# Optimization experiments

Measured on AMD Instinct MI355X. Metric: run time of the kernel, lower is better.

Reference implementation:

```python
import jax, jax.numpy as jnp
import numpy as np

# --- model hyperparameters (match init_kwargs / TrajectoryDecoder defaults) ---
R, T, KREG = 3, 16, 8          # num_radii, num_theta, reg_dim
RADIUS = 40.0                  # radius_scale
VEHICLE_HIDDEN = 16
MAP_HIDDEN = 8
IN_CH = VEHICLE_HIDDEN + MAP_HIDDEN  # 24
PREDICT_WINDOW = 30
TWO_PI = 2.0 * np.pi


def _reg_roll(f):
    # f: [..., C, k] -> [..., C, k(l), k(m)] with entry f[..., c, (m-l)%k]
    m = jnp.arange(KREG)[None, :]
    l = jnp.arange(KREG)[:, None]
    return f[..., (m - l) % KREG]


def _equilinear(W, f):
    # equivariant linear map between regular reps = circular (group) conv over reg dim
    # W: [out, in, k], f: [..., in, k] -> [..., out, k]
    return jnp.einsum('oil,...ilm->...om', W, _reg_roll(f))


def _reg2rho1(f, w):
    # frequency-1 Fourier projection of the regular rep -> rho1 (2-vector); 2 free params
    ang = TWO_PI * jnp.arange(KREG) / KREG
    c, s = jnp.cos(ang), jnp.sin(ang)
    W2 = jnp.stack([w[0] * c - w[1] * s, w[0] * s + w[1] * c], axis=-1)  # [k, 2]
    return jnp.einsum('...cm,md->...cd', f, W2)


def _cts_aggregate(dst_p, src_p, H, src_mask):
    # Continuous conv aggregation: bilinear interpolation of a polar-binned kernel
    # already contracted with source features.
    # H: [B, S, R, T, O, k] per-source, per-(radius,theta)-bin transformed features
    B, S, O = src_p.shape[0], src_p.shape[1], H.shape[-2]
    rel = src_p[:, None, :, :] - dst_p[:, :, None, :]      # [B, Nd, S, 2]
    d = jnp.sqrt(jnp.sum(rel * rel, axis=-1) + 1e-12)      # [B, Nd, S]
    valid = (d < RADIUS).astype(dst_p.dtype) * src_mask[:, None, :]
    win = jnp.maximum(1.0 - (d / RADIUS) ** 2, 0.0) ** 3   # CConv window
    cnt = jnp.maximum(jnp.sum(valid, axis=-1, keepdims=True), 1.0)
    base_w = valid * win / cnt
    # radial interpolation (clamped linear)
    u = jnp.clip(d / RADIUS, 0.0, 1.0) * (R - 1)
    r0f = jnp.floor(u); wr = u - r0f
    r0 = r0f.astype(jnp.int32); r1 = jnp.minimum(r0 + 1, R - 1)
    # angular interpolation (circular linear)
    t = ((jnp.arctan2(rel[..., 1], rel[..., 0]) / TWO_PI) % 1.0) * T
    t0f = jnp.floor(t); wt = t - t0f
    t0 = t0f.astype(jnp.int32) % T; t1 = (t0 + 1) % T
    Hf = H.reshape(B, S, R * T, O, KREG)
    bidx = jnp.arange(B)[:, None, None]
    sidx = jnp.arange(S)[None, None, :]
    out = jnp.zeros((B, dst_p.shape[1], O, KREG), dtype=dst_p.dtype)
    for ri, ti, cw in ((r0, t0, (1 - wr) * (1 - wt)),
                       (r0, t1, (1 - wr) * wt),
                       (r1, t0, wr * (1 - wt)),
                       (r1, t1, wr * wt)):
        g = Hf[bidx, sidx, ri * T + ti]                    # [B, Nd, S, O, k] irregular gather
        out = out + jnp.einsum('bns,bnsok->bnok', base_w * cw, g)
    return out


def _conv_reg(K, src_p, dst_p, f, src_mask):
    # EquiCtsConv2dRegToReg: per-bin group conv over reg dim, then continuous-conv gather
    H = jnp.einsum('rtoil,bsilm->bsrtom', K, _reg_roll(f))
    return _cts_aggregate(dst_p, src_p, H, src_mask)


def _conv_rho1(K, src_p, dst_p, v, src_mask):
    # EquiCtsConv2dRho1ToReg (in_channels=1): contract 2-vector input per bin
    H = jnp.einsum('rtomd,bsd->bsrtom', K, v)
    return _cts_aggregate(dst_p, src_p, H, src_mask)


def _decode(p, feat, car_mask, K_vehicle, Wd_vehicle, K_conv1, Wd1, K_conv2, Wd2):
    out = _conv_reg(K_vehicle, p, p, feat, car_mask) + _equilinear(Wd_vehicle, feat)
    for K, Wd in ((K_conv1, Wd1), (K_conv2, Wd2)):
        inf = jax.nn.relu(out)
        oc = _conv_reg(K, p, p, inf, car_mask)
        od = _equilinear(Wd, inf)
        out = oc + od + out if od.shape[-2] == out.shape[-2] else oc + od
    return jax.nn.relu(out)


def _forward(p, feat, map_p, map_feat, car_mask, map_mask,
             K_vehicle, Wd_vehicle, K_conv1, Wd1, K_conv2, Wd2,
             Wd_back, w_rho1, K_map):
    outputs = []
    output = _decode(p, feat, car_mask, K_vehicle, Wd_vehicle, K_conv1, Wd1, K_conv2, Wd2)
    delta = _reg2rho1(output, w_rho1)                      # [B, N, 3, 2]
    outputs.append(delta.at[..., 0, :].add(p))
    for _ in range(1, PREDICT_WINDOW):
        p = p + delta[..., 0, :]
        back = jnp.tanh(_equilinear(Wd_back, output))      # [B, N, 16, k]
        feat_v = feat[..., :VEHICLE_HIDDEN, :] * back
        enc = jax.nn.relu(_conv_rho1(K_map, map_p, p, map_feat, map_mask))  # MapEncoder
        feat = jnp.concatenate([feat_v, enc], axis=-2)     # [B, N, 24, k]
        output = _decode(p, feat, car_mask, K_vehicle, Wd_vehicle, K_conv1, Wd1, K_conv2, Wd2)
        delta = _reg2rho1(output, w_rho1)
        outputs.append(delta.at[..., 0, :].add(p))
    return jnp.stack(outputs, axis=0)                      # [30, B, N, 3, 2]


def setup_inputs() -> dict:
    key = jax.random.key(0)
    ks = jax.random.split(key, 13)
    B, N, M = 8, 64, 1024
    sc = 0.1
    return {
        'p': jax.random.normal(ks[0], (B, N, 2)) * 20.0,
        'feat': jax.random.normal(ks[1], (B, N, IN_CH, KREG)),
        'map_p': jax.random.normal(ks[2], (B, M, 2)) * 20.0,
        'map_feat': jax.random.normal(ks[3], (B, M, 2)),
        'car_mask': jnp.ones((B, N), dtype=jnp.float32),
        'map_mask': jnp.ones((B, M), dtype=jnp.float32),
        'K_vehicle': jax.random.normal(ks[4], (R, T, 8, IN_CH, KREG)) * sc,
        'Wd_vehicle': jax.random.normal(ks[5], (8, IN_CH, KREG)) * sc,
        'K_conv1': jax.random.normal(ks[6], (R, T, 8, 8, KREG)) * sc,
        'Wd1': jax.random.normal(ks[7], (8, 8, KREG)) * sc,
        'K_conv2': jax.random.normal(ks[8], (R, T, 3, 8, KREG)) * sc,
        'Wd2': jax.random.normal(ks[9], (3, 8, KREG)) * sc,
        'Wd_back': jax.random.normal(ks[10], (VEHICLE_HIDDEN, 3, KREG)) * sc,
        'w_rho1': jax.random.normal(ks[11], (2,)) * sc,
        'K_map': jax.random.normal(ks[12], (R, T, MAP_HIDDEN, KREG, 2)) * sc,
    }


def reference(p, feat, map_p, map_feat, car_mask, map_mask,
              K_vehicle, Wd_vehicle, K_conv1, Wd1, K_conv2, Wd2,
              Wd_back, w_rho1, K_map):
    return _forward(p, feat, map_p, map_feat, car_mask, map_mask,
                    K_vehicle, Wd_vehicle, K_conv1, Wd1, K_conv2, Wd2,
                    Wd_back, w_rho1, K_map)
```

## Files before the change

### kernel.cpp

```cpp
#include <hip/hip_runtime.h>
#include <math.h>

#define NB 8
#define NV 64
#define NM 1024
#define NR 3
#define NT 16
#define KR 8
#define RTOT 48
#define RADIUSF 40.0f
#define TWO_PIF 6.283185307179586f

__device__ __forceinline__ void pair_geom(float relx, float rely, float mask,
                                          float& valid, float& win,
                                          int bin[4], float cw[4]) {
    float d = sqrtf(relx * relx + rely * rely + 1e-12f);
    valid = (d < RADIUSF) ? mask : 0.0f;
    float q = d * (1.0f / RADIUSF);
    float w1 = fmaxf(1.0f - q * q, 0.0f);
    win = w1 * w1 * w1;
    float u = fminf(fmaxf(q, 0.0f), 1.0f) * (float)(NR - 1);
    float r0f = floorf(u);
    float wr = u - r0f;
    int r0 = (int)r0f;
    int r1 = min(r0 + 1, NR - 1);
    float a = atan2f(rely, relx) * (1.0f / TWO_PIF);
    a = a - floorf(a);
    float t = a * (float)NT;
    float t0f = floorf(t);
    float wt = t - t0f;
    int t0 = ((int)t0f) & (NT - 1);
    int t1 = (t0 + 1) & (NT - 1);
    bin[0] = r0 * NT + t0; cw[0] = (1.0f - wr) * (1.0f - wt);
    bin[1] = r0 * NT + t1; cw[1] = (1.0f - wr) * wt;
    bin[2] = r1 * NT + t0; cw[2] = wr * (1.0f - wt);
    bin[3] = r1 * NT + t1; cw[3] = wr * wt;
}

__global__ __launch_bounds__(64) void k_pairs0(const float* __restrict__ p,
                                               const float* __restrict__ car_mask,
                                               float* __restrict__ w4,
                                               int* __restrict__ bin4) {
    int b = blockIdx.x >> 6, n = blockIdx.x & 63;
    int s = threadIdx.x;
    float dx = p[(b * NV + n) * 2 + 0], dy = p[(b * NV + n) * 2 + 1];
    float relx = p[(b * NV + s) * 2 + 0] - dx;
    float rely = p[(b * NV + s) * 2 + 1] - dy;
    float valid, win; int bin[4]; float cw[4];
    pair_geom(relx, rely, car_mask[b * NV + s], valid, win, bin, cw);
    float c = valid;
#pragma unroll
    for (int off = 32; off > 0; off >>= 1) c += __shfl_xor(c, off);
    float bw = valid * win / fmaxf(c, 1.0f);
    int base = (blockIdx.x * NV + s) * 4;
#pragma unroll
    for (int q = 0; q < 4; ++q) { w4[base + q] = bw * cw[q]; bin4[base + q] = bin[q]; }
}

__global__ __launch_bounds__(256) void k_trans(
        const float* __restrict__ Kv, const float* __restrict__ K1g,
        const float* __restrict__ K2g, float4* __restrict__ KTv,
        float4* __restrict__ KT1, float4* __restrict__ KT2) {
    int idx = blockIdx.x * 256 + threadIdx.x;
    if (idx < 48 * 384) {
        int j = idx / 384, p = idx % 384;
        KTv[idx] = *(const float4*)(Kv + p * 192 + j * 4);
    } else if (idx < 48 * 384 + 16 * 384) {
        int r = idx - 48 * 384;
        int j = r / 384, p = r % 384;
        KT1[r] = *(const float4*)(K1g + p * 64 + j * 4);
    } else if (idx < 48 * 384 + 16 * 384 + 16 * 144) {
        int r = idx - (48 * 384 + 16 * 384);
        int j = r / 144, p = r % 144;
        KT2[r] = *(const float4*)(K2g + p * 64 + j * 4);
    }
}

__global__ __launch_bounds__(256) void k_H0(const float* __restrict__ inb,
        const float4* __restrict__ KT, float* __restrict__ H) {
    __shared__ __align__(16) float s_f[192];
    int bs = blockIdx.x, tid = threadIdx.x;
    if (tid < 192) s_f[tid] = inb[bs * 192 + tid];
    __syncthreads();
    for (int p = tid; p < 384; p += 256) {
        float acc[KR];
#pragma unroll
        for (int m = 0; m < KR; ++m) acc[m] = 0.f;
#pragma unroll 8
        for (int i = 0; i < 24; ++i) {
            float4 k0 = KT[(2 * i) * 384 + p];
            float4 k1 = KT[(2 * i + 1) * 384 + p];
            float kk[8] = {k0.x, k0.y, k0.z, k0.w, k1.x, k1.y, k1.z, k1.w};
            float ff[8];
            *(float4*)&ff[0] = *(const float4*)&s_f[i * 8];
            *(float4*)&ff[4] = *(const float4*)&s_f[i * 8 + 4];
#pragma unroll
            for (int l = 0; l < KR; ++l) {
                float kl = kk[l];
#pragma unroll
                for (int m = 0; m < KR; ++m)
                    acc[m] = fmaf(kl, ff[(m - l) & 7], acc[m]);
            }
        }
        int rt = p >> 3, o = p & 7;
        float* hr = H + (size_t)(bs * RTOT + rt) * 64 + o * KR;
#pragma unroll
        for (int m = 0; m < KR; ++m) hr[m] = acc[m];
    }
}

__global__ __launch_bounds__(256) void k_advHv(int t,
        const float* __restrict__ pprev, float* __restrict__ pcur,
        const float* __restrict__ outD, float* __restrict__ feat,
        const float* __restrict__ w_rho1, const float* __restrict__ WdBack,
        const float* __restrict__ Kmap, const float* __restrict__ map_p,
        const float* __restrict__ map_feat, const float* __restrict__ map_mask,
        const float* __restrict__ car_mask,
        float* __restrict__ w4, int* __restrict__ bin4,
        float* __restrict__ out,
        const float4* __restrict__ KTv, float* __restrict__ Hv) {
    __shared__ float s_out0[NV * KR];
    __shared__ float s_own[3 * KR];
    __shared__ float s_psrc[NV * 2];
    __shared__ float s_G4[4 * 96];
    __shared__ float s_G[96];
    __shared__ float s_wred[4];
    __shared__ float s_w2[KR * 2];
    __shared__ __align__(16) float s_f2[192];

    int tid = threadIdx.x;
    int bn = blockIdx.x, b = bn >> 6, n = bn & 63;

    for (int i = tid; i < NV * KR; i += 256)
        s_out0[i] = outD[(b * NV + (i >> 3)) * 24 + (i & 7)];
    if (tid < 24) s_own[tid] = outD[(b * NV + n) * 24 + tid];
    if (tid >= 32 && tid < 48) {
        int r = tid - 32, m = r >> 1, dd = r & 1;
        float ang = TWO_PIF * (float)m / (float)KR;
        float sn, cs; sincosf(ang, &sn, &cs);
        float w0 = w_rho1[0], wq = w_rho1[1];
        s_w2[r] = (dd == 0) ? (w0 * cs - wq * sn) : (w0 * sn + wq * cs);
    }
    if (tid < 96) { s_G4[tid] = 0.f; s_G4[96 + tid] = 0.f; s_G4[192 + tid] = 0.f; s_G4[288 + tid] = 0.f; }
    __syncthreads();

    if (tid < NV) {
        int s = tid;
        float dx0 = 0.0f, dy0 = 0.0f;
#pragma unroll
        for (int m = 0; m < KR; ++m) {
            float v = s_out0[s * KR + m];
            dx0 = fmaf(v, s_w2[m * 2 + 0], dx0);
            dy0 = fmaf(v, s_w2[m * 2 + 1], dy0);
        }
        s_psrc[s * 2 + 0] = pprev[(b * NV + s) * 2 + 0] + dx0;
        s_psrc[s * 2 + 1] = pprev[(b * NV + s) * 2 + 1] + dy0;
    }
    if (tid >= 64 && tid < 70) {
        int r = tid - 64, c = r >> 1, dd = r & 1;
        float acc = 0.0f;
#pragma unroll
        for (int m = 0; m < KR; ++m)
            acc = fmaf(s_own[c * KR + m], s_w2[m * 2 + dd], acc);
        if (c == 0) acc += pprev[(b * NV + n) * 2 + dd];
        out[(((t - 1) * NB + b) * NV + n) * 6 + c * 2 + dd] = acc;
    }
    __syncthreads();
    if (tid < 2) pcur[(b * NV + n) * 2 + tid] = s_psrc[n * 2 + tid];

    float pdx = s_psrc[n * 2 + 0], pdy = s_psrc[n * 2 + 1];

    if (tid < NV) {
        int s = tid;
        float valid, win; int bin[4]; float cw[4];
        pair_geom(s_psrc[s * 2 + 0] - pdx, s_psrc[s * 2 + 1] - pdy,
                  car_mask[b * NV + s], valid, win, bin, cw);
        float c = valid;
#pragma unroll
        for (int off = 32; off > 0; off >>= 1) c += __shfl_xor(c, off);
        float bw = valid * win / fmaxf(c, 1.0f);
        int base = (bn * NV + s) * 4;
#pragma unroll
        for (int q = 0; q < 4; ++q) { w4[base + q] = bw * cw[q]; bin4[base + q] = bin[q]; }
    }

    float lc = 0.0f;
    float* myG = &s_G4[(tid >> 6) * 96];
#pragma unroll
    for (int j = 0; j < NM / 256; ++j) {
        int s = tid + j * 256;
        float2 mp = *(const float2*)&map_p[(b * NM + s) * 2];
        float valid, win; int bin[4]; float cw[4];
        pair_geom(mp.x - pdx, mp.y - pdy, map_mask[b * NM + s], valid, win, bin, cw);
        lc += valid;
        float ww = valid * win;
        if (ww > 0.0f) {
            float2 f2 = *(const float2*)&map_feat[(b * NM + s) * 2];
#pragma unroll
            for (int q = 0; q < 4; ++q) {
                float w = ww * cw[q];
                atomicAdd(&myG[bin[q] * 2 + 0], w * f2.x);
                atomicAdd(&myG[bin[q] * 2 + 1], w * f2.y);
            }
        }
    }
#pragma unroll
    for (int off = 32; off > 0; off >>= 1) lc += __shfl_xor(lc, off);
    if ((tid & 63) == 0) s_wred[tid >> 6] = lc;
    __syncthreads();
    if (tid < 96) s_G[tid] = s_G4[tid] + s_G4[96 + tid] + s_G4[192 + tid] + s_G4[288 + tid];
    __syncthreads();
    float invc = 1.0f / fmaxf(s_wred[0] + s_wred[1] + s_wred[2] + s_wred[3], 1.0f);

    if (tid < 64) {
        float acc = 0.0f;
#pragma unroll 8
        for (int rt = 0; rt < RTOT; ++rt) {
            float2 k2 = *(const float2*)&Kmap[(rt * 64 + tid) * 2];
            acc = fmaf(k2.x, s_G[rt * 2 + 0], acc);
            acc = fmaf(k2.y, s_G[rt * 2 + 1], acc);
        }
        s_f2[128 + tid] = fmaxf(acc * invc, 0.0f);
    }
    if (tid >= 128) {
        int r = tid - 128, i = r >> 3, m = r & 7;
        float acc = 0.0f;
#pragma unroll
        for (int c = 0; c < 3; ++c)
#pragma unroll
            for (int l = 0; l < KR; ++l)
                acc = fmaf(WdBack[(i * 3 + c) * 8 + l], s_own[c * 8 + ((m - l) & 7)], acc);
        s_f2[r] = feat[(b * NV + n) * 192 + r] * tanhf(acc);
    }
    __syncthreads();
    if (tid < 192) feat[bn * 192 + tid] = s_f2[tid];

    for (int p = tid; p < 384; p += 256) {
        float acc[KR];
#pragma unroll
        for (int m = 0; m < KR; ++m) acc[m] = 0.f;
#pragma unroll 8
        for (int i = 0; i < 24; ++i) {
            float4 k0 = KTv[(2 * i) * 384 + p];
            float4 k1 = KTv[(2 * i + 1) * 384 + p];
            float kk[8] = {k0.x, k0.y, k0.z, k0.w, k1.x, k1.y, k1.z, k1.w};
            float ff[8];
            *(float4*)&ff[0] = *(const float4*)&s_f2[i * 8];
            *(float4*)&ff[4] = *(const float4*)&s_f2[i * 8 + 4];
#pragma unroll
            for (int l = 0; l < KR; ++l) {
                float kl = kk[l];
#pragma unroll
                for (int m = 0; m < KR; ++m)
                    acc[m] = fmaf(kl, ff[(m - l) & 7], acc[m]);
            }
        }
        int rt = p >> 3, o = p & 7;
        float* hr = Hv + (size_t)(bn * RTOT + rt) * 64 + o * KR;
#pragma unroll
        for (int m = 0; m < KR; ++m) hr[m] = acc[m];
    }
}

template<int ICH, bool RELU_IN, bool RESID, int OCH2>
__global__ __launch_bounds__(256) void k_aggH(const float* __restrict__ inb,
        const float* __restrict__ H, const float* __restrict__ Wd,
        const float* __restrict__ w4, const int* __restrict__ bin4,
        const float4* __restrict__ KT2, float* __restrict__ outb,
        float* __restrict__ Hout) {
    constexpr int NC = ICH * KR;
    constexpr int HS = 64;
    constexpr int NPAIR2 = RTOT * OCH2;
    constexpr int HS2 = OCH2 * KR;
    __shared__ float s_w[256];
    __shared__ int   s_row[256];
    __shared__ float s_in[NC];
    __shared__ __align__(16) float s_part[16 * HS];
    __shared__ __align__(16) float s_f2[HS];
    int tid = threadIdx.x, bn = blockIdx.x, b = bn >> 6;
    s_w[tid] = w4[bn * 256 + tid];
    s_row[tid] = (b * NV + (tid >> 2)) * RTOT + bin4[bn * 256 + tid];
    if (tid < NC) s_in[tid] = inb[bn * NC + tid];
    __syncthreads();
    {
        int w = tid >> 6, lane = tid & 63;
        int g = lane >> 4, c4 = lane & 15;
        float4 acc = make_float4(0.f, 0.f, 0.f, 0.f);
#pragma unroll
        for (int j = 0; j < 16; ++j) {
            int idx = w * 64 + j * 4 + g;
            float we = s_w[idx];
            float4 v = *(const float4*)&H[(size_t)s_row[idx] * HS + c4 * 4];
            acc.x = fmaf(we, v.x, acc.x);
            acc.y = fmaf(we, v.y, acc.y);
            acc.z = fmaf(we, v.z, acc.z);
            acc.w = fmaf(we, v.w, acc.w);
        }
        *(float4*)&s_part[(w * 4 + g) * HS + c4 * 4] = acc;
    }
    __syncthreads();
    if (tid < HS) {
        float tot = 0.f;
#pragma unroll
        for (int k = 0; k < 16; ++k) tot += s_part[k * HS + tid];
        int o = tid / KR, m = tid & 7;
#pragma unroll
        for (int i = 0; i < ICH; ++i) {
            const float* Wr = Wd + (o * ICH + i) * KR;
#pragma unroll
            for (int l = 0; l < KR; ++l) {
                float v = s_in[i * KR + ((m - l) & 7)];
                if (RELU_IN) v = fmaxf(v, 0.f);
                tot = fmaf(Wr[l], v, tot);
            }
        }
        if (RESID) tot += s_in[tid];
        outb[bn * HS + tid] = tot;
        s_f2[tid] = fmaxf(tot, 0.f);
    }
    __syncthreads();
    for (int p = tid; p < NPAIR2; p += 256) {
        float acc2[KR];
#pragma unroll
        for (int m = 0; m < KR; ++m) acc2[m] = 0.f;
#pragma unroll 4
        for (int i = 0; i < 8; ++i) {
            float4 k0 = KT2[(2 * i) * NPAIR2 + p];
            float4 k1 = KT2[(2 * i + 1) * NPAIR2 + p];
            float kk[8] = {k0.x, k0.y, k0.z, k0.w, k1.x, k1.y, k1.z, k1.w};
            float ff[8];
            *(float4*)&ff[0] = *(const float4*)&s_f2[i * 8];
            *(float4*)&ff[4] = *(const float4*)&s_f2[i * 8 + 4];
#pragma unroll
            for (int l = 0; l < KR; ++l) {
                float kl = kk[l];
#pragma unroll
                for (int m = 0; m < KR; ++m)
                    acc2[m] = fmaf(kl, ff[(m - l) & 7], acc2[m]);
            }
        }
        int rt = p / OCH2, o = p - rt * OCH2;
        float* hr = Hout + (size_t)(bn * RTOT + rt) * HS2 + o * KR;
#pragma unroll
        for (int m = 0; m < KR; ++m) hr[m] = acc2[m];
    }
}

__global__ __launch_bounds__(256) void k_agg3(const float* __restrict__ inb,
        const float* __restrict__ H, const float* __restrict__ Wd,
        const float* __restrict__ w4, const int* __restrict__ bin4,
        float* __restrict__ outb) {
    constexpr int NC = 64;
    constexpr int HS = 24;
    __shared__ float s_w[256];
    __shared__ int   s_row[256];
    __shared__ float s_in[NC];
    __shared__ __align__(16) float s_part[32 * HS];
    int tid = threadIdx.x, bn = blockIdx.x, b = bn >> 6;
    s_w[tid] = w4[bn * 256 + tid];
    s_row[tid] = (b * NV + (tid >> 2)) * RTOT + bin4[bn * 256 + tid];
    if (tid < NC) s_in[tid] = inb[bn * NC + tid];
    __syncthreads();
    {
        int w = tid >> 6, lane = tid & 63;
        int g = lane >> 3, c4 = lane & 7;
        float4 acc = make_float4(0.f, 0.f, 0.f, 0.f);
#pragma unroll
        for (int j = 0; j < 8; ++j) {
            int idx = w * 64 + j * 8 + g;
            float we = s_w[idx];
            if (c4 < 6) {
                float4 v = *(const float4*)&H[(size_t)s_row[idx] * HS + c4 * 4];
                acc.x = fmaf(we, v.x, acc.x);
                acc.y = fmaf(we, v.y, acc.y);
                acc.z = fmaf(we, v.z, acc.z);
                acc.w = fmaf(we, v.w, acc.w);
            }
        }
        if (c4 < 6) *(float4*)&s_part[(w * 8 + g) * HS + c4 * 4] = acc;
    }
    __syncthreads();
    if (tid < HS) {
        float tot = 0.f;
#pragma unroll
        for (int k = 0; k < 32; ++k) tot += s_part[k * HS + tid];
        int o = tid / KR, m = tid & 7;
#pragma unroll
        for (int i = 0; i < 8; ++i) {
            const float* Wr = Wd + (o * 8 + i) * KR;
#pragma unroll
            for (int l = 0; l < KR; ++l)
                tot = fmaf(Wr[l], fmaxf(s_in[i * KR + ((m - l) & 7)], 0.f), tot);
        }
        outb[bn * HS + tid] = fmaxf(tot, 0.f);
    }
}

__global__ void k_final(const float* __restrict__ outD, const float* __restrict__ pcur,
                        const float* __restrict__ w_rho1, float* __restrict__ out) {
    int idx = blockIdx.x * blockDim.x + threadIdx.x;
    if (idx >= NB * NV * 6) return;
    int bn = idx / 6, r = idx % 6, c = r >> 1, dd = r & 1;
    float w0 = w_rho1[0], wq = w_rho1[1];
    float acc = 0.0f;
#pragma unroll
    for (int m = 0; m < KR; ++m) {
        float ang = TWO_PIF * (float)m / (float)KR;
        float sn, cs; sincosf(ang, &sn, &cs);
        float w2 = (dd == 0) ? (w0 * cs - wq * sn) : (w0 * sn + wq * cs);
        acc = fmaf(outD[bn * 24 + c * 8 + m], w2, acc);
    }
    if (c == 0) acc += pcur[bn * 2 + dd];
    out[(29 * NB * NV + bn) * 6 + r] = acc;
}

extern "C" void kernel_launch(void* const* d_in, const int* in_sizes, int n_in,
                              void* d_out, int out_size, void* d_ws, size_t ws_size,
                              hipStream_t stream) {
    const float* in_p     = (const float*)d_in[0];
    const float* in_feat  = (const float*)d_in[1];
    const float* map_p    = (const float*)d_in[2];
    const float* map_feat = (const float*)d_in[3];
    const float* car_mask = (const float*)d_in[4];
    const float* map_mask = (const float*)d_in[5];
    const float* Kv       = (const float*)d_in[6];
    const float* WdV      = (const float*)d_in[7];
    const float* K1       = (const float*)d_in[8];
    const float* Wd1      = (const float*)d_in[9];
    const float* K2       = (const float*)d_in[10];
    const float* Wd2      = (const float*)d_in[11];
    const float* WdBack   = (const float*)d_in[12];
    const float* w_rho1   = (const float*)d_in[13];
    const float* Kmap     = (const float*)d_in[14];

    float* ws   = (float*)d_ws;
    float* pbuf0 = ws;
    float* pbuf1 = ws + 1024;
    float* feat  = ws + 2048;
    float* out1  = ws + 100352;
    float* out2  = ws + 133120;
    float* outD  = ws + 165888;
    float* w4    = ws + 178176;
    int*   bin4  = (int*)(ws + 309248);
    float4* KTv  = (float4*)(ws + 440320);
    float4* KT1  = (float4*)(ws + 514048);
    float4* KT2  = (float4*)(ws + 538624);
    float* Hv    = ws + 547840;
    float* H1    = ws + 2120704;
    float* H2    = ws + 3693568;
    float* out   = (float*)d_out;

    hipMemcpyAsync(pbuf0, in_p, NB * NV * 2 * sizeof(float),
                   hipMemcpyDeviceToDevice, stream);
    hipMemcpyAsync(feat, in_feat, NB * NV * 24 * KR * sizeof(float),
                   hipMemcpyDeviceToDevice, stream);

    k_trans<<<105, 256, 0, stream>>>(Kv, K1, K2, KTv, KT1, KT2);
    k_pairs0<<<NB * NV, 64, 0, stream>>>(pbuf0, car_mask, w4, bin4);

    auto decode = [&]() {
        k_aggH<24, false, false, 8><<<NB * NV, 256, 0, stream>>>(feat, Hv, WdV, w4, bin4, KT1, out1, H1);
        k_aggH<8, true, true, 3><<<NB * NV, 256, 0, stream>>>(out1, H1, Wd1, w4, bin4, KT2, out2, H2);
        k_agg3<<<NB * NV, 256, 0, stream>>>(out2, H2, Wd2, w4, bin4, outD);
    };

    k_H0<<<NB * NV, 256, 0, stream>>>(feat, KTv, Hv);
    decode();
    for (int t = 1; t < 30; ++t) {
        float* pprev = (t & 1) ? pbuf0 : pbuf1;
        float* pcur  = (t & 1) ? pbuf1 : pbuf0;
        k_advHv<<<NB * NV, 256, 0, stream>>>(t, pprev, pcur, outD, feat,
                                             w_rho1, WdBack, Kmap, map_p, map_feat,
                                             map_mask, car_mask, w4, bin4, out,
                                             KTv, Hv);
        decode();
    }
    k_final<<<12, 256, 0, stream>>>(outD, pbuf1, w_rho1, out);
}
```

Measured before the change: 1.765 ms.

## Fuse stage-3 aggregation into advance kernel and pair geometry into first decode stage

After: 1.744 ms. Within noise of the previous version (-1.2%).

```diff
diff --git a/kernel.cpp b/kernel.cpp
--- a/kernel.cpp
+++ b/kernel.cpp
@@ -37,26 +37,6 @@
     bin[3] = r1 * NT + t1; cw[3] = wr * wt;
 }
 
-__global__ __launch_bounds__(64) void k_pairs0(const float* __restrict__ p,
-                                               const float* __restrict__ car_mask,
-                                               float* __restrict__ w4,
-                                               int* __restrict__ bin4) {
-    int b = blockIdx.x >> 6, n = blockIdx.x & 63;
-    int s = threadIdx.x;
-    float dx = p[(b * NV + n) * 2 + 0], dy = p[(b * NV + n) * 2 + 1];
-    float relx = p[(b * NV + s) * 2 + 0] - dx;
-    float rely = p[(b * NV + s) * 2 + 1] - dy;
-    float valid, win; int bin[4]; float cw[4];
-    pair_geom(relx, rely, car_mask[b * NV + s], valid, win, bin, cw);
-    float c = valid;
-#pragma unroll
-    for (int off = 32; off > 0; off >>= 1) c += __shfl_xor(c, off);
-    float bw = valid * win / fmaxf(c, 1.0f);
-    int base = (blockIdx.x * NV + s) * 4;
-#pragma unroll
-    for (int q = 0; q < 4; ++q) { w4[base + q] = bw * cw[q]; bin4[base + q] = bin[q]; }
-}
-
 __global__ __launch_bounds__(256) void k_trans(
         const float* __restrict__ Kv, const float* __restrict__ K1g,
         const float* __restrict__ K2g, float4* __restrict__ KTv,
@@ -109,33 +89,35 @@
     }
 }
 
-__global__ __launch_bounds__(256) void k_advHv(int t,
-        const float* __restrict__ pprev, float* __restrict__ pcur,
-        const float* __restrict__ outD, float* __restrict__ feat,
+__global__ __launch_bounds__(256) void k_A(int t,
+        float* __restrict__ p, const float* __restrict__ out2buf,
+        const float* __restrict__ H2, const float* __restrict__ Wd2,
+        const float* __restrict__ w4, const int* __restrict__ bin4,
+        float* __restrict__ feat,
         const float* __restrict__ w_rho1, const float* __restrict__ WdBack,
         const float* __restrict__ Kmap, const float* __restrict__ map_p,
         const float* __restrict__ map_feat, const float* __restrict__ map_mask,
-        const float* __restrict__ car_mask,
-        float* __restrict__ w4, int* __restrict__ bin4,
-        float* __restrict__ out,
-        const float4* __restrict__ KTv, float* __restrict__ Hv) {
-    __shared__ float s_out0[NV * KR];
-    __shared__ float s_own[3 * KR];
-    __shared__ float s_psrc[NV * 2];
+        const float4* __restrict__ KTv, float* __restrict__ Hv,
+        float* __restrict__ out) {
+    __shared__ float s_w[256];
+    __shared__ int   s_row[256];
+    __shared__ float s_in[64];
+    __shared__ __align__(16) float s_part[32 * 24];
+    __shared__ float s_oD[24];
+    __shared__ float s_w2[16];
     __shared__ float s_G4[4 * 96];
     __shared__ float s_G[96];
     __shared__ float s_wred[4];
-    __shared__ float s_w2[KR * 2];
     __shared__ __align__(16) float s_f2[192];
 
-    int tid = threadIdx.x;
-    int bn = blockIdx.x, b = bn >> 6, n = bn & 63;
-
-    for (int i = tid; i < NV * KR; i += 256)
-        s_out0[i] = outD[(b * NV + (i >> 3)) * 24 + (i & 7)];
-    if (tid < 24) s_own[tid] = outD[(b * NV + n) * 24 + tid];
-    if (tid >= 32 && tid < 48) {
-        int r = tid - 32, m = r >> 1, dd = r & 1;
+    int tid = threadIdx.x, bn = blockIdx.x, b = bn >> 6, n = bn & 63;
+    float2 pold = *(const float2*)&p[bn * 2];
+
+    s_w[tid] = w4[bn * 256 + tid];
+    s_row[tid] = (b * NV + (tid >> 2)) * RTOT + bin4[bn * 256 + tid];
+    if (tid < 64) s_in[tid] = out2buf[bn * 64 + tid];
+    if (tid >= 224 && tid < 240) {
+        int r = tid - 224, m = r >> 1, dd = r & 1;
         float ang = TWO_PIF * (float)m / (float)KR;
         float sn, cs; sincosf(ang, &sn, &cs);
         float w0 = w_rho1[0], wq = w_rho1[1];
@@ -144,47 +126,61 @@
     if (tid < 96) { s_G4[tid] = 0.f; s_G4[96 + tid] = 0.f; s_G4[192 + tid] = 0.f; s_G4[288 + tid] = 0.f; }
     __syncthreads();
 
-    if (tid < NV) {
-        int s = tid;
-        float dx0 = 0.0f, dy0 = 0.0f;
-#pragma unroll
-        for (int m = 0; m < KR; ++m) {
-            float v = s_out0[s * KR + m];
-            dx0 = fmaf(v, s_w2[m * 2 + 0], dx0);
-            dy0 = fmaf(v, s_w2[m * 2 + 1], dy0);
-        }
-        s_psrc[s * 2 + 0] = pprev[(b * NV + s) * 2 + 0] + dx0;
-        s_psrc[s * 2 + 1] = pprev[(b * NV + s) * 2 + 1] + dy0;
-    }
-    if (tid >= 64 && tid < 70) {
-        int r = tid - 64, c = r >> 1, dd = r & 1;
-        float acc = 0.0f;
+    {
+        int w = tid >> 6, lane = tid & 63;
+        int g = lane >> 3, c4 = lane & 7;
+        float4 acc = make_float4(0.f, 0.f, 0.f, 0.f);
+#pragma unroll
+        for (int j = 0; j < 8; ++j) {
+            int idx = w * 64 + j * 8 + g;
+            float we = s_w[idx];
+            if (c4 < 6) {
+                float4 v = *(const float4*)&H2[(size_t)s_row[idx] * 24 + c4 * 4];
+                acc.x = fmaf(we, v.x, acc.x);
+                acc.y = fmaf(we, v.y, acc.y);
+                acc.z = fmaf(we, v.z, acc.z);
+                acc.w = fmaf(we, v.w, acc.w);
+            }
+        }
+        if (c4 < 6) *(float4*)&s_part[(w * 8 + g) * 24 + c4 * 4] = acc;
+    }
+    __syncthreads();
+    if (tid < 24) {
+        float tot = 0.f;
+#pragma unroll
+        for (int k = 0; k < 32; ++k) tot += s_part[k * 24 + tid];
+        int o = tid / KR, m = tid & 7;
+#pragma unroll
+        for (int i = 0; i < 8; ++i) {
+            const float* Wr = Wd2 + (o * 8 + i) * KR;
+#pragma unroll
+            for (int l = 0; l < KR; ++l)
+                tot = fmaf(Wr[l], fmaxf(s_in[i * KR + ((m - l) & 7)], 0.f), tot);
+        }
+        s_oD[tid] = fmaxf(tot, 0.f);
+    }
+    __syncthreads();
+
+    float dx0 = 0.f, dy0 = 0.f;
+#pragma unroll
+    for (int m = 0; m < KR; ++m) {
+        float v = s_oD[m];
+        dx0 = fmaf(v, s_w2[m * 2 + 0], dx0);
+        dy0 = fmaf(v, s_w2[m * 2 + 1], dy0);
+    }
+    if (tid < 6) {
+        int c = tid >> 1, dd = tid & 1;
+        float acc = 0.f;
 #pragma unroll
         for (int m = 0; m < KR; ++m)
-            acc = fmaf(s_own[c * KR + m], s_w2[m * 2 + dd], acc);
-        if (c == 0) acc += pprev[(b * NV + n) * 2 + dd];
-        out[(((t - 1) * NB + b) * NV + n) * 6 + c * 2 + dd] = acc;
-    }
-    __syncthreads();
-    if (tid < 2) pcur[(b * NV + n) * 2 + tid] = s_psrc[n * 2 + tid];
-
-    float pdx = s_psrc[n * 2 + 0], pdy = s_psrc[n * 2 + 1];
-
-    if (tid < NV) {
-        int s = tid;
-        float valid, win; int bin[4]; float cw[4];
-        pair_geom(s_psrc[s * 2 + 0] - pdx, s_psrc[s * 2 + 1] - pdy,
-                  car_mask[b * NV + s], valid, win, bin, cw);
-        float c = valid;
-#pragma unroll
-        for (int off = 32; off > 0; off >>= 1) c += __shfl_xor(c, off);
-        float bw = valid * win / fmaxf(c, 1.0f);
-        int base = (bn * NV + s) * 4;
-#pragma unroll
-        for (int q = 0; q < 4; ++q) { w4[base + q] = bw * cw[q]; bin4[base + q] = bin[q]; }
-    }
-
-    float lc = 0.0f;
+            acc = fmaf(s_oD[c * KR + m], s_w2[m * 2 + dd], acc);
+        if (c == 0) acc += (dd ? pold.y : pold.x);
+        out[(((t - 1) * NB + b) * NV + n) * 6 + tid] = acc;
+    }
+    float pdx = pold.x + dx0, pdy = pold.y + dy0;
+    if (tid == 0) { p[bn * 2 + 0] = pdx; p[bn * 2 + 1] = pdy; }
+
+    float lc = 0.f;
     float* myG = &s_G4[(tid >> 6) * 96];
 #pragma unroll
     for (int j = 0; j < NM / 256; ++j) {
@@ -194,7 +190,7 @@
         pair_geom(mp.x - pdx, mp.y - pdy, map_mask[b * NM + s], valid, win, bin, cw);
         lc += valid;
         float ww = valid * win;
-        if (ww > 0.0f) {
+        if (ww > 0.f) {
             float2 f2 = *(const float2*)&map_feat[(b * NM + s) * 2];
 #pragma unroll
             for (int q = 0; q < 4; ++q) {
@@ -213,36 +209,36 @@
     float invc = 1.0f / fmaxf(s_wred[0] + s_wred[1] + s_wred[2] + s_wred[3], 1.0f);
 
     if (tid < 64) {
-        float acc = 0.0f;
+        float acc = 0.f;
 #pragma unroll 8
         for (int rt = 0; rt < RTOT; ++rt) {
             float2 k2 = *(const float2*)&Kmap[(rt * 64 + tid) * 2];
             acc = fmaf(k2.x, s_G[rt * 2 + 0], acc);
             acc = fmaf(k2.y, s_G[rt * 2 + 1], acc);
         }
-        s_f2[128 + tid] = fmaxf(acc * invc, 0.0f);
+        s_f2[128 + tid] = fmaxf(acc * invc, 0.f);
     }
     if (tid >= 128) {
         int r = tid - 128, i = r >> 3, m = r & 7;
-        float acc = 0.0f;
+        float acc = 0.f;
 #pragma unroll
         for (int c = 0; c < 3; ++c)
 #pragma unroll
             for (int l = 0; l < KR; ++l)
-                acc = fmaf(WdBack[(i * 3 + c) * 8 + l], s_own[c * 8 + ((m - l) & 7)], acc);
-        s_f2[r] = feat[(b * NV + n) * 192 + r] * tanhf(acc);
+                acc = fmaf(WdBack[(i * 3 + c) * 8 + l], s_oD[c * 8 + ((m - l) & 7)], acc);
+        s_f2[r] = feat[bn * 192 + r] * tanhf(acc);
     }
     __syncthreads();
     if (tid < 192) feat[bn * 192 + tid] = s_f2[tid];
 
-    for (int p = tid; p < 384; p += 256) {
+    for (int pp = tid; pp < 384; pp += 256) {
         float acc[KR];
 #pragma unroll
         for (int m = 0; m < KR; ++m) acc[m] = 0.f;
 #pragma unroll 8
         for (int i = 0; i < 24; ++i) {
-            float4 k0 = KTv[(2 * i) * 384 + p];
-            float4 k1 = KTv[(2 * i + 1) * 384 + p];
+            float4 k0 = KTv[(2 * i) * 384 + pp];
+            float4 k1 = KTv[(2 * i + 1) * 384 + pp];
             float kk[8] = {k0.x, k0.y, k0.z, k0.w, k1.x, k1.y, k1.z, k1.w};
             float ff[8];
             *(float4*)&ff[0] = *(const float4*)&s_f2[i * 8];
@@ -255,32 +251,49 @@
                     acc[m] = fmaf(kl, ff[(m - l) & 7], acc[m]);
             }
         }
-        int rt = p >> 3, o = p & 7;
+        int rt = pp >> 3, o = pp & 7;
         float* hr = Hv + (size_t)(bn * RTOT + rt) * 64 + o * KR;
 #pragma unroll
         for (int m = 0; m < KR; ++m) hr[m] = acc[m];
     }
 }
 
-template<int ICH, bool RELU_IN, bool RESID, int OCH2>
-__global__ __launch_bounds__(256) void k_aggH(const float* __restrict__ inb,
-        const float* __restrict__ H, const float* __restrict__ Wd,
-        const float* __restrict__ w4, const int* __restrict__ bin4,
-        const float4* __restrict__ KT2, float* __restrict__ outb,
-        float* __restrict__ Hout) {
-    constexpr int NC = ICH * KR;
-    constexpr int HS = 64;
-    constexpr int NPAIR2 = RTOT * OCH2;
-    constexpr int HS2 = OCH2 * KR;
+__global__ __launch_bounds__(256) void k_B(
+        const float* __restrict__ p, const float* __restrict__ car_mask,
+        const float* __restrict__ feat, const float* __restrict__ Hv,
+        const float* __restrict__ WdV,
+        float* __restrict__ w4, int* __restrict__ bin4,
+        const float4* __restrict__ KT1,
+        float* __restrict__ out1, float* __restrict__ H1) {
+    __shared__ float s_psrc[NV * 2];
     __shared__ float s_w[256];
     __shared__ int   s_row[256];
-    __shared__ float s_in[NC];
-    __shared__ __align__(16) float s_part[16 * HS];
-    __shared__ __align__(16) float s_f2[HS];
-    int tid = threadIdx.x, bn = blockIdx.x, b = bn >> 6;
-    s_w[tid] = w4[bn * 256 + tid];
-    s_row[tid] = (b * NV + (tid >> 2)) * RTOT + bin4[bn * 256 + tid];
-    if (tid < NC) s_in[tid] = inb[bn * NC + tid];
+    __shared__ __align__(16) float s_in[192];
+    __shared__ __align__(16) float s_part[16 * 64];
+    __shared__ __align__(16) float s_f2[64];
+    int tid = threadIdx.x, bn = blockIdx.x, b = bn >> 6, n = bn & 63;
+    if (tid < 128) s_psrc[tid] = p[b * 128 + tid];
+    if (tid < 192) s_in[tid] = feat[bn * 192 + tid];
+    __syncthreads();
+    if (tid < NV) {
+        int s = tid;
+        float valid, win; int bin[4]; float cw[4];
+        pair_geom(s_psrc[s * 2 + 0] - s_psrc[n * 2 + 0],
+                  s_psrc[s * 2 + 1] - s_psrc[n * 2 + 1],
+                  car_mask[b * NV + s], valid, win, bin, cw);
+        float c = valid;
+#pragma unroll
+        for (int off = 32; off > 0; off >>= 1) c += __shfl_xor(c, off);
+        float bw = valid * win / fmaxf(c, 1.0f);
+#pragma unroll
+        for (int q = 0; q < 4; ++q) {
+            float wv = bw * cw[q];
+            s_w[s * 4 + q] = wv;
+            s_row[s * 4 + q] = (b * NV + s) * RTOT + bin[q];
+            w4[bn * 256 + s * 4 + q] = wv;
+            bin4[bn * 256 + s * 4 + q] = bin[q];
+        }
+    }
     __syncthreads();
     {
         int w = tid >> 6, lane = tid & 63;
@@ -290,43 +303,39 @@
         for (int j = 0; j < 16; ++j) {
             int idx = w * 64 + j * 4 + g;
             float we = s_w[idx];
-            float4 v = *(const float4*)&H[(size_t)s_row[idx] * HS + c4 * 4];
+            float4 v = *(const float4*)&Hv[(size_t)s_row[idx] * 64 + c4 * 4];
             acc.x = fmaf(we, v.x, acc.x);
             acc.y = fmaf(we, v.y, acc.y);
             acc.z = fmaf(we, v.z, acc.z);
             acc.w = fmaf(we, v.w, acc.w);
         }
-        *(float4*)&s_part[(w * 4 + g) * HS + c4 * 4] = acc;
-    }
-    __syncthreads();
-    if (tid < HS) {
+        *(float4*)&s_part[(w * 4 + g) * 64 + c4 * 4] = acc;
+    }
+    __syncthreads();
+    if (tid < 64) {
         float tot = 0.f;
 #pragma unroll
-        for (int k = 0; k < 16; ++k) tot += s_part[k * HS + tid];
-        int o = tid / KR, m = tid & 7;
-#pragma unroll
-        for (int i = 0; i < ICH; ++i) {
-            const float* Wr = Wd + (o * ICH + i) * KR;
-#pragma unroll
-            for (int l = 0; l < KR; ++l) {
-                float v = s_in[i * KR + ((m - l) & 7)];
-                if (RELU_IN) v = fmaxf(v, 0.f);
-                tot = fmaf(Wr[l], v, tot);
-            }
-        }
-        if (RESID) tot += s_in[tid];
-        outb[bn * HS + tid] = tot;
+        for (int k = 0; k < 16; ++k) tot += s_part[k * 64 + tid];
+        int o = tid >> 3, m = tid & 7;
+#pragma unroll
+        for (int i = 0; i < 24; ++i) {
+            const float* Wr = WdV + (o * 24 + i) * KR;
+#pragma unroll
+            for (int l = 0; l < KR; ++l)
+                tot = fmaf(Wr[l], s_in[i * KR + ((m - l) & 7)], tot);
+        }
+        out1[bn * 64 + tid] = tot;
         s_f2[tid] = fmaxf(tot, 0.f);
     }
     __syncthreads();
-    for (int p = tid; p < NPAIR2; p += 256) {
+    for (int pp = tid; pp < 384; pp += 256) {
         float acc2[KR];
 #pragma unroll
         for (int m = 0; m < KR; ++m) acc2[m] = 0.f;
 #pragma unroll 4
         for (int i = 0; i < 8; ++i) {
-            float4 k0 = KT2[(2 * i) * NPAIR2 + p];
-            float4 k1 = KT2[(2 * i + 1) * NPAIR2 + p];
+            float4 k0 = KT1[(2 * i) * 384 + pp];
+            float4 k1 = KT1[(2 * i + 1) * 384 + pp];
             float kk[8] = {k0.x, k0.y, k0.z, k0.w, k1.x, k1.y, k1.z, k1.w};
             float ff[8];
             *(float4*)&ff[0] = *(const float4*)&s_f2[i * 8];
@@ -339,27 +348,111 @@
                     acc2[m] = fmaf(kl, ff[(m - l) & 7], acc2[m]);
             }
         }
-        int rt = p / OCH2, o = p - rt * OCH2;
-        float* hr = Hout + (size_t)(bn * RTOT + rt) * HS2 + o * KR;
+        int rt = pp >> 3, o = pp & 7;
+        float* hr = H1 + (size_t)(bn * RTOT + rt) * 64 + o * KR;
 #pragma unroll
         for (int m = 0; m < KR; ++m) hr[m] = acc2[m];
     }
 }
 
-__global__ __launch_bounds__(256) void k_agg3(const float* __restrict__ inb,
-        const float* __restrict__ H, const float* __restrict__ Wd,
+__global__ __launch_bounds__(256) void k_C(const float* __restrict__ out1,
+        const float* __restrict__ H1, const float* __restrict__ Wd1,
         const float* __restrict__ w4, const int* __restrict__ bin4,
-        float* __restrict__ outb) {
-    constexpr int NC = 64;
-    constexpr int HS = 24;
+        const float4* __restrict__ KT2, float* __restrict__ out2,
+        float* __restrict__ H2) {
     __shared__ float s_w[256];
     __shared__ int   s_row[256];
-    __shared__ float s_in[NC];
-    __shared__ __align__(16) float s_part[32 * HS];
+    __shared__ float s_in[64];
+    __shared__ __align__(16) float s_part[16 * 64];
+    __shared__ __align__(16) float s_f2[64];
     int tid = threadIdx.x, bn = blockIdx.x, b = bn >> 6;
     s_w[tid] = w4[bn * 256 + tid];
     s_row[tid] = (b * NV + (tid >> 2)) * RTOT + bin4[bn * 256 + tid];
-    if (tid < NC) s_in[tid] = inb[bn * NC + tid];
+    if (tid < 64) s_in[tid] = out1[bn * 64 + tid];
+    __syncthreads();
+    {
+        int w = tid >> 6, lane = tid & 63;
+        int g = lane >> 4, c4 = lane & 15;
+        float4 acc = make_float4(0.f, 0.f, 0.f, 0.f);
+#pragma unroll
+        for (int j = 0; j < 16; ++j) {
+            int idx = w * 64 + j * 4 + g;
+            float we = s_w[idx];
+            float4 v = *(const float4*)&H1[(size_t)s_row[idx] * 64 + c4 * 4];
+            acc.x = fmaf(we, v.x, acc.x);
+            acc.y = fmaf(we, v.y, acc.y);
+            acc.z = fmaf(we, v.z, acc.z);
+            acc.w = fmaf(we, v.w, acc.w);
+        }
+        *(float4*)&s_part[(w * 4 + g) * 64 + c4 * 4] = acc;
+    }
+    __syncthreads();
+    if (tid < 64) {
+        float tot = 0.f;
+#pragma unroll
+        for (int k = 0; k < 16; ++k) tot += s_part[k * 64 + tid];
+        int o = tid >> 3, m = tid & 7;
+#pragma unroll
+        for (int i = 0; i < 8; ++i) {
+            const float* Wr = Wd1 + (o * 8 + i) * KR;
+#pragma unroll
+            for (int l = 0; l < KR; ++l)
+                tot = fmaf(Wr[l], fmaxf(s_in[i * KR + ((m - l) & 7)], 0.f), tot);
+        }
+        tot += s_in[tid];
+        out2[bn * 64 + tid] = tot;
+        s_f2[tid] = fmaxf(tot, 0.f);
+    }
+    __syncthreads();
+    for (int pp = tid; pp < 144; pp += 256) {
+        float acc2[KR];
+#pragma unroll
+        for (int m = 0; m < KR; ++m) acc2[m] = 0.f;
+#pragma unroll 4
+        for (int i = 0; i < 8; ++i) {
+            float4 k0 = KT2[(2 * i) * 144 + pp];
+            float4 k1 = KT2[(2 * i + 1) * 144 + pp];
+            float kk[8] = {k0.x, k0.y, k0.z, k0.w, k1.x, k1.y, k1.z, k1.w};
+            float ff[8];
+            *(float4*)&ff[0] = *(const float4*)&s_f2[i * 8];
+            *(float4*)&ff[4] = *(const float4*)&s_f2[i * 8 + 4];
+#pragma unroll
+            for (int l = 0; l < KR; ++l) {
+                float kl = kk[l];
+#pragma unroll
+                for (int m = 0; m < KR; ++m)
+                    acc2[m] = fmaf(kl, ff[(m - l) & 7], acc2[m]);
+            }
+        }
+        int rt = pp / 3, o = pp - rt * 3;
+        float* hr = H2 + (size_t)(bn * RTOT + rt) * 24 + o * KR;
+#pragma unroll
+        for (int m = 0; m < KR; ++m) hr[m] = acc2[m];
+    }
+}
+
+__global__ __launch_bounds__(256) void k_fin(
+        const float* __restrict__ p, const float* __restrict__ out2buf,
+        const float* __restrict__ H2, const float* __restrict__ Wd2,
+        const float* __restrict__ w4, const int* __restrict__ bin4,
+        const float* __restrict__ w_rho1, float* __restrict__ out) {
+    __shared__ float s_w[256];
+    __shared__ int   s_row[256];
+    __shared__ float s_in[64];
+    __shared__ __align__(16) float s_part[32 * 24];
+    __shared__ float s_oD[24];
+    __shared__ float s_w2[16];
+    int tid = threadIdx.x, bn = blockIdx.x, b = bn >> 6, n = bn & 63;
+    s_w[tid] = w4[bn * 256 + tid];
+    s_row[tid] = (b * NV + (tid >> 2)) * RTOT + bin4[bn * 256 + tid];
+    if (tid < 64) s_in[tid] = out2buf[bn * 64 + tid];
+    if (tid >= 224 && tid < 240) {
+        int r = tid - 224, m = r >> 1, dd = r & 1;
+        float ang = TWO_PIF * (float)m / (float)KR;
+        float sn, cs; sincosf(ang, &sn, &cs);
+        float w0 = w_rho1[0], wq = w_rho1[1];
+        s_w2[r] = (dd == 0) ? (w0 * cs - wq * sn) : (w0 * sn + wq * cs);
+    }
     __syncthreads();
     {
         int w = tid >> 6, lane = tid & 63;
@@ -370,48 +463,40 @@
             int idx = w * 64 + j * 8 + g;
             float we = s_w[idx];
             if (c4 < 6) {
-                float4 v = *(const float4*)&H[(size_t)s_row[idx] * HS + c4 * 4];
+                float4 v = *(const float4*)&H2[(size_t)s_row[idx] * 24 + c4 * 4];
                 acc.x = fmaf(we, v.x, acc.x);
                 acc.y = fmaf(we, v.y, acc.y);
                 acc.z = fmaf(we, v.z, acc.z);
                 acc.w = fmaf(we, v.w, acc.w);
             }
         }
-        if (c4 < 6) *(float4*)&s_part[(w * 8 + g) * HS + c4 * 4] = acc;
-    }
-    __syncthreads();
-    if (tid < HS) {
+        if (c4 < 6) *(float4*)&s_part[(w * 8 + g) * 24 + c4 * 4] = acc;
+    }
+    __syncthreads();
+    if (tid < 24) {
         float tot = 0.f;
 #pragma unroll
-        for (int k = 0; k < 32; ++k) tot += s_part[k * HS + tid];
+        for (int k = 0; k < 32; ++k) tot += s_part[k * 24 + tid];
         int o = tid / KR, m = tid & 7;
 #pragma unroll
         for (int i = 0; i < 8; ++i) {
-            const float* Wr = Wd + (o * 8 + i) * KR;
+            const float* Wr = Wd2 + (o * 8 + i) * KR;
 #pragma unroll
             for (int l = 0; l < KR; ++l)
                 tot = fmaf(Wr[l], fmaxf(s_in[i * KR + ((m - l) & 7)], 0.f), tot);
         }
-        outb[bn * HS + tid] = fmaxf(tot, 0.f);
-    }
-}
-
-__global__ void k_final(const float* __restrict__ outD, const float* __restrict__ pcur,
-                        const float* __restrict__ w_rho1, float* __restrict__ out) {
-    int idx = blockIdx.x * blockDim.x + threadIdx.x;
-    if (idx >= NB * NV * 6) return;
-    int bn = idx / 6, r = idx % 6, c = r >> 1, dd = r & 1;
-    float w0 = w_rho1[0], wq = w_rho1[1];
-    float acc = 0.0f;
-#pragma unroll
-    for (int m = 0; m < KR; ++m) {
-        float ang = TWO_PIF * (float)m / (float)KR;
-        float sn, cs; sincosf(ang, &sn, &cs);
-        float w2 = (dd == 0) ? (w0 * cs - wq * sn) : (w0 * sn + wq * cs);
-        acc = fmaf(outD[bn * 24 + c * 8 + m], w2, acc);
-    }
-    if (c == 0) acc += pcur[bn * 2 + dd];
-    out[(29 * NB * NV + bn) * 6 + r] = acc;
+        s_oD[tid] = fmaxf(tot, 0.f);
+    }
+    __syncthreads();
+    if (tid < 6) {
+        int c = tid >> 1, dd = tid & 1;
+        float acc = 0.f;
+#pragma unroll
+        for (int m = 0; m < KR; ++m)
+            acc = fmaf(s_oD[c * KR + m], s_w2[m * 2 + dd], acc);
+        if (c == 0) acc += p[bn * 2 + dd];
+        out[((29 * NB + b) * NV + n) * 6 + tid] = acc;
+    }
 }
 
 extern "C" void kernel_launch(void* const* d_in, const int* in_sizes, int n_in,
@@ -434,12 +519,10 @@
     const float* Kmap     = (const float*)d_in[14];
 
     float* ws   = (float*)d_ws;
-    float* pbuf0 = ws;
-    float* pbuf1 = ws + 1024;
+    float* pbuf  = ws;
     float* feat  = ws + 2048;
     float* out1  = ws + 100352;
     float* out2  = ws + 133120;
-    float* outD  = ws + 165888;
     float* w4    = ws + 178176;
     int*   bin4  = (int*)(ws + 309248);
     float4* KTv  = (float4*)(ws + 440320);
@@ -450,30 +533,23 @@
     float* H2    = ws + 3693568;
     float* out   = (float*)d_out;
 
-    hipMemcpyAsync(pbuf0, in_p, NB * NV * 2 * sizeof(float),
+    hipMemcpyAsync(pbuf, in_p, NB * NV * 2 * sizeof(float),
                    hipMemcpyDeviceToDevice, stream);
     hipMemcpyAsync(feat, in_feat, NB * NV * 24 * KR * sizeof(float),
                    hipMemcpyDeviceToDevice, stream);
 
     k_trans<<<105, 256, 0, stream>>>(Kv, K1, K2, KTv, KT1, KT2);
-    k_pairs0<<<NB * NV, 64, 0, stream>>>(pbuf0, car_mask, w4, bin4);
-
-    auto decode = [&]() {
-        k_aggH<24, false, false, 8><<<NB * NV, 256, 0, stream>>>(feat, Hv, WdV, w4, bin4, KT1, out1, H1);
-        k_aggH<8, true, true, 3><<<NB * NV, 256, 0, stream>>>(out1, H1, Wd1, w4, bin4, KT2, out2, H2);
-        k_agg3<<<NB * NV, 256, 0, stream>>>(out2, H2, Wd2, w4, bin4, outD);
-    };
-
     k_H0<<<NB * NV, 256, 0, stream>>>(feat, KTv, Hv);
-    decode();
+
+    k_B<<<NB * NV, 256, 0, stream>>>(pbuf, car_mask, feat, Hv, WdV, w4, bin4, KT1, out1, H1);
+    k_C<<<NB * NV, 256, 0, stream>>>(out1, H1, Wd1, w4, bin4, KT2, out2, H2);
+
     for (int t = 1; t < 30; ++t) {
-        float* pprev = (t & 1) ? pbuf0 : pbuf1;
-        float* pcur  = (t & 1) ? pbuf1 : pbuf0;
-        k_advHv<<<NB * NV, 256, 0, stream>>>(t, pprev, pcur, outD, feat,
-                                             w_rho1, WdBack, Kmap, map_p, map_feat,
-                                             map_mask, car_mask, w4, bin4, out,
-                                             KTv, Hv);
-        decode();
-    }
-    k_final<<<12, 256, 0, stream>>>(outD, pbuf1, w_rho1, out);
-}
+        k_A<<<NB * NV, 256, 0, stream>>>(t, pbuf, out2, H2, Wd2, w4, bin4, feat,
+                                         w_rho1, WdBack, Kmap, map_p, map_feat,
+                                         map_mask, KTv, Hv, out);
+        k_B<<<NB * NV, 256, 0, stream>>>(pbuf, car_mask, feat, Hv, WdV, w4, bin4, KT1, out1, H1);
+        k_C<<<NB * NV, 256, 0, stream>>>(out1, H1, Wd1, w4, bin4, KT2, out2, H2);
+    }
+    k_fin<<<NB * NV, 256, 0, stream>>>(pbuf, out2, H2, Wd2, w4, bin4, w_rho1, out);
+}
```
